# Optimization experiments

Measured on AMD Instinct MI355X. Metric: run time of the kernel, lower is better.

The kernel has to match this reference:

```python
import jax, jax.numpy as jnp
import numpy as np

HEADS = 8
DIM_HEAD = 64
QLEVEL = 127.0  # symmetric int8: clamp to [-128, 127]


def fake_quant(x):
    """Symmetric per-tensor int8 fake quantization with straight-through estimator."""
    delta = jnp.max(jnp.abs(x)) / QLEVEL
    xq = jnp.clip(jnp.round(x / delta), -128.0, 127.0) * delta
    return x + jax.lax.stop_gradient(xq - x)


def setup_inputs() -> dict:
    key = jax.random.key(0)
    ks = jax.random.split(key, 7)
    b, n, m, d, dc = 2, 4096, 1024, 512, 768
    return {
        "x": jax.random.normal(ks[0], (b, n, d), jnp.float32),
        "context": jax.random.normal(ks[1], (b, m, dc), jnp.float32),
        "Wq": jax.random.normal(ks[2], (d, d), jnp.float32) * 0.02,
        "Wk": jax.random.normal(ks[3], (dc, d), jnp.float32) * 0.02,
        "Wv": jax.random.normal(ks[4], (dc, d), jnp.float32) * 0.02,
        "Wo": jax.random.normal(ks[5], (d, d), jnp.float32) * 0.02,
        "bo": jnp.zeros((d,), jnp.float32),
    }


def reference(x, context, Wq, Wk, Wv, Wo, bo):
    b, n, _ = x.shape
    h, dh = HEADS, DIM_HEAD
    scale = dh ** -0.5

    q = x @ Wq            # [b, n, h*dh]
    k = context @ Wk      # [b, m, h*dh]
    v = context @ Wv      # [b, m, h*dh]

    def split(t):  # b n (h d) -> b h n d
        return t.reshape(t.shape[0], t.shape[1], h, dh).transpose(0, 2, 1, 3)

    q, k, v = split(q), split(k), split(v)

    # fake-quantize q and k before the score matmul (use_aq=True path)
    q = fake_quant(q)
    k = fake_quant(k)
    sim = jnp.einsum('bhid,bhjd->bhij', q, k) * scale  # [b, h, n, m]
    attn = jax.nn.softmax(sim, axis=-1)

    # fake-quantize attention weights and v before the AV matmul
    out = jnp.einsum('bhij,bhjd->bhid', fake_quant(attn), fake_quant(v))
    out = out.transpose(0, 2, 1, 3).reshape(b, n, h * dh)  # b h n d -> b n (h d)
    return out @ Wo + bo  # to_out[0]; to_out[-1] is Dropout (identity in eval)
```

## Files before the change

### kernel.cpp

```cpp
#include <hip/hip_runtime.h>
#include <stdint.h>

typedef float  v4f  __attribute__((ext_vector_type(4)));
typedef int    v4i  __attribute__((ext_vector_type(4)));
typedef __bf16 v8bf __attribute__((ext_vector_type(8)));
typedef __bf16 v4bf __attribute__((ext_vector_type(4)));

#define BATCH  2
#define NQ     4096
#define MK     1024
#define DMODEL 512
#define DCTX   768
#define NH     8
#define DH     64

__global__ __launch_bounds__(256) void k_wtrans(
    const float* __restrict__ Wq, const float* __restrict__ Wk,
    const float* __restrict__ Wv, const float* __restrict__ Wo,
    __bf16* __restrict__ Wq_t, __bf16* __restrict__ Wk_t,
    __bf16* __restrict__ Wv_t, __bf16* __restrict__ Wo_t,
    unsigned* __restrict__ scal) {
  if (blockIdx.x == 0 && blockIdx.y == 0 && blockIdx.z == 0 && threadIdx.x < 4)
    scal[threadIdx.x] = 0u;
  const float* src; __bf16* dst; int K;
  switch (blockIdx.z) {
    case 0:  src = Wq; dst = Wq_t; K = DMODEL; break;
    case 1:  src = Wk; dst = Wk_t; K = DCTX;   break;
    case 2:  src = Wv; dst = Wv_t; K = DCTX;   break;
    default: src = Wo; dst = Wo_t; K = DMODEL; break;
  }
  int k0 = blockIdx.y * 32;
  if (k0 >= K) return;
  int n0 = blockIdx.x * 32;
  __shared__ __bf16 tile[32][33];
  int c = threadIdx.x & 31, r0 = threadIdx.x >> 5;
  for (int i = 0; i < 4; ++i) {
    int r = r0 + i * 8;
    tile[c][r] = (__bf16)src[(size_t)(k0 + r) * DMODEL + n0 + c];
  }
  __syncthreads();
  for (int i = 0; i < 4; ++i) {
    int r = r0 + i * 8;
    dst[(size_t)(n0 + r) * K + k0 + c] = tile[r][c];
  }
}

__global__ __launch_bounds__(256) void k_cvt(
    const float* __restrict__ x, const float* __restrict__ ctx,
    __bf16* __restrict__ xb, __bf16* __restrict__ cb) {
  const int XC = BATCH * NQ * DMODEL / 8;
  const int CC = BATCH * MK * DCTX / 8;
  int idx = blockIdx.x * 256 + threadIdx.x;
  const float* src; __bf16* dst;
  if (idx < XC) { src = x + (size_t)idx * 8; dst = xb + (size_t)idx * 8; }
  else {
    int j = idx - XC;
    if (j >= CC) return;
    src = ctx + (size_t)j * 8; dst = cb + (size_t)j * 8;
  }
  float4 a = *(const float4*)src, b = *(const float4*)(src + 4);
  v8bf o = { (__bf16)a.x, (__bf16)a.y, (__bf16)a.z, (__bf16)a.w,
             (__bf16)b.x, (__bf16)b.y, (__bf16)b.z, (__bf16)b.w };
  *(v8bf*)dst = o;
}

template<int K_, bool BIAS, bool AMAX>
__global__ __launch_bounds__(256, 3) void k_gemm_bs(
    const __bf16* __restrict__ A, const __bf16* __restrict__ Bt,
    float* __restrict__ C, int M, int N,
    const float* __restrict__ bias,
    unsigned* __restrict__ amaxLo, unsigned* __restrict__ amaxHi) {
  constexpr int CS = K_ + 8;
  constexpr int GPC = K_ / 8;
  __shared__ __bf16 Bs[32 * CS];
  __shared__ float redmax[4];
  const int tid = threadIdx.x;
  const int lane = tid & 63, wave = tid >> 6;
  const int l15 = lane & 15, g = lane >> 4;
  const int col0 = blockIdx.y * 32;
  const int row0w = blockIdx.x * 128 + wave * 32;

#pragma unroll
  for (int i = 0; i < GPC * 32 / 256; ++i) {
    int f = i * 256 + tid;
    int c = f / GPC, w = f - c * GPC;
    *(v8bf*)(&Bs[c * CS + w * 8]) =
        *(const v8bf*)(Bt + (size_t)(col0 + c) * K_ + w * 8);
  }
  __syncthreads();

  v4f acc[2][2] = {};
  const __bf16* a0 = A + (size_t)(row0w + l15) * K_ + g * 8;
  const __bf16* a1 = A + (size_t)(row0w + 16 + l15) * K_ + g * 8;
#pragma unroll
  for (int k0 = 0; k0 < K_; k0 += 32) {
    v8bf af0 = *(const v8bf*)(a0 + k0);
    v8bf af1 = *(const v8bf*)(a1 + k0);
    v8bf bf0 = *(const v8bf*)(&Bs[l15 * CS + k0 + g * 8]);
    v8bf bf1 = *(const v8bf*)(&Bs[(16 + l15) * CS + k0 + g * 8]);
    acc[0][0] = __builtin_amdgcn_mfma_f32_16x16x32_bf16(af0, bf0, acc[0][0], 0, 0, 0);
    acc[0][1] = __builtin_amdgcn_mfma_f32_16x16x32_bf16(af0, bf1, acc[0][1], 0, 0, 0);
    acc[1][0] = __builtin_amdgcn_mfma_f32_16x16x32_bf16(af1, bf0, acc[1][0], 0, 0, 0);
    acc[1][1] = __builtin_amdgcn_mfma_f32_16x16x32_bf16(af1, bf1, acc[1][1], 0, 0, 0);
  }

  float lmax = 0.0f;
#pragma unroll
  for (int j = 0; j < 2; ++j) {
    int col = col0 + j * 16 + l15;
    float bv = BIAS ? bias[col] : 0.0f;
#pragma unroll
    for (int i = 0; i < 2; ++i) {
#pragma unroll
      for (int r = 0; r < 4; ++r) {
        int row = row0w + i * 16 + g * 4 + r;
        float cv = acc[i][j][r] + bv;
        C[(size_t)row * N + col] = cv;
        if (AMAX) lmax = fmaxf(lmax, fabsf(cv));
      }
    }
  }
  if (AMAX) {
    for (int off = 32; off > 0; off >>= 1)
      lmax = fmaxf(lmax, __shfl_xor(lmax, off, 64));
    if (lane == 0) redmax[wave] = lmax;
    __syncthreads();
    if (tid == 0) {
      float bm = fmaxf(fmaxf(redmax[0], redmax[1]), fmaxf(redmax[2], redmax[3]));
      atomicMax(col0 < 512 ? amaxLo : amaxHi, __float_as_uint(bm));
    }
  }
}

__global__ __launch_bounds__(256) void k_quant_kv(
    const float* __restrict__ kvf,
    int8_t* __restrict__ k8, int8_t* __restrict__ v8t,
    const unsigned* __restrict__ scal) {
  __shared__ int8_t tile[64][80];
  int bx = blockIdx.x;
  if (bx < 1024) {
    int j = bx * 256 + threadIdx.x;
    int r = j >> 7;
    int c4 = (j & 127) << 2;
    float4 v = *(const float4*)(kvf + (size_t)r * 1024 + c4);
    float s = 127.0f / __uint_as_float(scal[1]);
    int a0 = __float2int_rn(v.x * s), a1 = __float2int_rn(v.y * s);
    int a2 = __float2int_rn(v.z * s), a3 = __float2int_rn(v.w * s);
    a0 = max(-128, min(127, a0)); a1 = max(-128, min(127, a1));
    a2 = max(-128, min(127, a2)); a3 = max(-128, min(127, a3));
    unsigned p = (unsigned)(a0 & 255) | ((unsigned)(a1 & 255) << 8) |
                 ((unsigned)(a2 & 255) << 16) | ((unsigned)(a3 & 255) << 24);
    *(unsigned*)(k8 + (size_t)j * 4) = p;
    return;
  }
  int id = bx - 1024;
  int bh = id >> 4, b = bh >> 3, h = bh & 7;
  int j0 = (id & 15) * 64;
  const float s = 127.0f / __uint_as_float(scal[2]);
  int t = threadIdx.x;
  int j = t >> 2, dh0 = (t & 3) << 4;
  const float* src = kvf + (size_t)(b * MK + j0 + j) * 1024 + 512 + h * DH + dh0;
#pragma unroll
  for (int i = 0; i < 16; i += 4) {
    float4 v = *(const float4*)(src + i);
    int a0 = __float2int_rn(v.x * s), a1 = __float2int_rn(v.y * s);
    int a2 = __float2int_rn(v.z * s), a3 = __float2int_rn(v.w * s);
    tile[dh0 + i + 0][j] = (int8_t)max(-128, min(127, a0));
    tile[dh0 + i + 1][j] = (int8_t)max(-128, min(127, a1));
    tile[dh0 + i + 2][j] = (int8_t)max(-128, min(127, a2));
    tile[dh0 + i + 3][j] = (int8_t)max(-128, min(127, a3));
  }
  __syncthreads();
  int dh = t >> 2, jb = (t & 3) << 4;
  v4i val = *(const v4i*)(&tile[dh][jb]);
  *(v4i*)(v8t + (size_t)(bh * DH + dh) * MK + j0 + jb) = val;
}

__device__ __forceinline__ v4i quant_pack16(const float* p, float s) {
  v4i out;
#pragma unroll
  for (int q = 0; q < 4; ++q) {
    float4 v = *(const float4*)(p + q * 4);
    int a0 = __float2int_rn(v.x * s), a1 = __float2int_rn(v.y * s);
    int a2 = __float2int_rn(v.z * s), a3 = __float2int_rn(v.w * s);
    a0 = max(-128, min(127, a0)); a1 = max(-128, min(127, a1));
    a2 = max(-128, min(127, a2)); a3 = max(-128, min(127, a3));
    out[q] = (int)((unsigned)(a0 & 255) | ((unsigned)(a1 & 255) << 8) |
                   ((unsigned)(a2 & 255) << 16) | ((unsigned)(a3 & 255) << 24));
  }
  return out;
}

__global__ __launch_bounds__(256, 4) void k_pass1(
    const float* __restrict__ qf, int8_t* __restrict__ q8,
    const int8_t* __restrict__ k8,
    float* __restrict__ invz, unsigned* __restrict__ scal) {
  __shared__ __align__(16) int8_t kbuf[128 * 72];
  __shared__ float mared[4];
  int bh = blockIdx.y, b = bh >> 3, h = bh & 7;
  int wave = threadIdx.x >> 6, lane = threadIdx.x & 63;
  int l15 = lane & 15, g = lane >> 4;
  int row0 = blockIdx.x * 64;
  int myrow = row0 + wave * 16 + l15;
  const float aq = __uint_as_float(scal[0]), ak = __uint_as_float(scal[1]);
  const float alpha2 = (aq * ak) * (0.125f / (127.0f * 127.0f)) * 1.44269504f;
  const float sq = 127.0f / aq;
  const v4i z4 = {0, 0, 0, 0};
  size_t qoff = (size_t)(b * NQ + myrow) * DMODEL + h * DH + g * 16;
  v4i qfrag = quant_pack16(qf + qoff, sq);
  *(v4i*)(q8 + qoff) = qfrag;
  const int8_t* kbase = k8 + (size_t)b * MK * DMODEL + h * DH;
  const int rs = threadIdx.x >> 2, qs = (threadIdx.x & 3) * 16;

  float z[4] = {0.f, 0.f, 0.f, 0.f};
  int mi = -(1 << 30);
  for (int tile = 0; tile < 8; ++tile) {
    __syncthreads();
    *(v4i*)(&kbuf[rs * 72 + qs]) =
        *(const v4i*)(kbase + (size_t)(tile * 128 + rs) * DMODEL + qs);
    *(v4i*)(&kbuf[(rs + 64) * 72 + qs]) =
        *(const v4i*)(kbase + (size_t)(tile * 128 + rs + 64) * DMODEL + qs);
    __syncthreads();
    float zt = z[tile >> 1];
#pragma unroll
    for (int t = 0; t < 8; ++t) {
      v4i kfrag = *(const v4i*)(&kbuf[(t * 16 + l15) * 72 + g * 16]);
      v4i sa = __builtin_amdgcn_mfma_i32_16x16x64_i8(kfrag, qfrag, z4, 0, 0, 0);
      mi = max(mi, max(max(sa[0], sa[1]), max(sa[2], sa[3])));
      float e0 = __builtin_amdgcn_exp2f((float)sa[0] * alpha2);
      float e1 = __builtin_amdgcn_exp2f((float)sa[1] * alpha2);
      float e2 = __builtin_amdgcn_exp2f((float)sa[2] * alpha2);
      float e3 = __builtin_amdgcn_exp2f((float)sa[3] * alpha2);
      zt += (e0 + e1) + (e2 + e3);
    }
    z[tile >> 1] = zt;
  }
#pragma unroll
  for (int i = 0; i < 4; ++i) {
    z[i] += __shfl_xor(z[i], 16, 64);
    z[i] += __shfl_xor(z[i], 32, 64);
  }
  mi = max(mi, __shfl_xor(mi, 16, 64));
  mi = max(mi, __shfl_xor(mi, 32, 64));
  float zt = (z[0] + z[1]) + (z[2] + z[3]);
  float iz = 1.0f / zt;
  if (g == 0) invz[(size_t)bh * NQ + myrow] = iz;
  float ma = __builtin_amdgcn_exp2f((float)mi * alpha2) * iz;
#pragma unroll
  for (int off = 1; off < 16; off <<= 1)
    ma = fmaxf(ma, __shfl_xor(ma, off, 64));
  if (lane == 0) mared[wave] = ma;
  __syncthreads();
  if (threadIdx.x == 0)
    atomicMax(scal + 3,
              __float_as_uint(fmaxf(fmaxf(mared[0], mared[1]),
                                    fmaxf(mared[2], mared[3]))));
}

__global__ __launch_bounds__(256, 4) void k_pass2(
    const int8_t* __restrict__ q8, const int8_t* __restrict__ k8,
    const int8_t* __restrict__ v8t, const float* __restrict__ invz,
    const unsigned* __restrict__ scal, __bf16* __restrict__ o) {
  __shared__ __align__(16) int8_t kbuf[128 * 72];
  __shared__ __align__(16) int8_t vbuf[64 * 152];
  __shared__ __align__(16) int8_t albuf[4][16 * 152];
  int bh = blockIdx.y, b = bh >> 3, h = bh & 7;
  int wave = threadIdx.x >> 6, lane = threadIdx.x & 63;
  int l15 = lane & 15, g = lane >> 4;
  int row0 = blockIdx.x * 64;
  int myrow = row0 + wave * 16 + l15;
  const float aq = __uint_as_float(scal[0]), ak = __uint_as_float(scal[1]);
  const float avv = __uint_as_float(scal[2]), izm = __uint_as_float(scal[3]);
  const float alpha2 = (aq * ak) * (0.125f / (127.0f * 127.0f)) * 1.44269504f;
  const float oscale = (izm / 127.0f) * (avv / 127.0f);
  const float MAGIC = 12582912.0f;
  const v4i z4 = {0, 0, 0, 0};

  v4i qfrag = *(const v4i*)(q8 + (size_t)(b * NQ + myrow) * DMODEL + h * DH + g * 16);
  const float lcr = __builtin_amdgcn_logf(invz[(size_t)bh * NQ + myrow] * (127.0f / izm));
  const int8_t* kbase = k8 + (size_t)b * MK * DMODEL + h * DH;
  const int8_t* vbase = v8t + (size_t)bh * DH * MK;
  int8_t* alds = albuf[wave];
  const int rs = threadIdx.x >> 2, qs = (threadIdx.x & 3) * 16;
  const int vr = threadIdx.x >> 3, vq = (threadIdx.x & 7) * 16;

  v4i pacc[4] = {};
  for (int tile = 0; tile < 8; ++tile) {
    __syncthreads();
    *(v4i*)(&kbuf[rs * 72 + qs]) =
        *(const v4i*)(kbase + (size_t)(tile * 128 + rs) * DMODEL + qs);
    *(v4i*)(&kbuf[(rs + 64) * 72 + qs]) =
        *(const v4i*)(kbase + (size_t)(tile * 128 + rs + 64) * DMODEL + qs);
    *(v4i*)(&vbuf[vr * 152 + vq]) =
        *(const v4i*)(vbase + (size_t)vr * MK + tile * 128 + vq);
    *(v4i*)(&vbuf[(vr + 32) * 152 + vq]) =
        *(const v4i*)(vbase + (size_t)(vr + 32) * MK + tile * 128 + vq);
    __syncthreads();
#pragma unroll
    for (int t = 0; t < 8; ++t) {
      v4i kfrag = *(const v4i*)(&kbuf[(t * 16 + l15) * 72 + g * 16]);
      v4i sa = __builtin_amdgcn_mfma_i32_16x16x64_i8(kfrag, qfrag, z4, 0, 0, 0);
      float f0 = __builtin_amdgcn_exp2f(fmaf((float)sa[0], alpha2, lcr)) + MAGIC;
      float f1 = __builtin_amdgcn_exp2f(fmaf((float)sa[1], alpha2, lcr)) + MAGIC;
      float f2 = __builtin_amdgcn_exp2f(fmaf((float)sa[2], alpha2, lcr)) + MAGIC;
      float f3 = __builtin_amdgcn_exp2f(fmaf((float)sa[3], alpha2, lcr)) + MAGIC;
      unsigned packed = (__float_as_uint(f0) & 255u) |
                        ((__float_as_uint(f1) & 255u) << 8) |
                        ((__float_as_uint(f2) & 255u) << 16) |
                        (__float_as_uint(f3) << 24);
      *(unsigned*)(alds + l15 * 152 + t * 16 + g * 4) = packed;
    }
#pragma unroll
    for (int c = 0; c < 2; ++c) {
      v4i afrag = *(const v4i*)(alds + l15 * 152 + c * 64 + g * 16);
#pragma unroll
      for (int d = 0; d < 4; ++d) {
        v4i bfrag = *(const v4i*)(&vbuf[(d * 16 + l15) * 152 + c * 64 + g * 16]);
        pacc[d] = __builtin_amdgcn_mfma_i32_16x16x64_i8(afrag, bfrag, pacc[d], 0, 0, 0);
      }
    }
  }
  __bf16* obase = o + (size_t)(b * NQ + row0 + wave * 16) * DMODEL + h * DH;
#pragma unroll
  for (int d = 0; d < 4; ++d)
#pragma unroll
    for (int r = 0; r < 4; ++r)
      obase[(size_t)(g * 4 + r) * DMODEL + d * 16 + l15] =
          (__bf16)((float)pacc[d][r] * oscale);
}

extern "C" void kernel_launch(void* const* d_in, const int* in_sizes, int n_in,
                              void* d_out, int out_size, void* d_ws, size_t ws_size,
                              hipStream_t stream) {
  (void)in_sizes; (void)n_in; (void)out_size; (void)ws_size;
  const float* x   = (const float*)d_in[0];
  const float* ctx = (const float*)d_in[1];
  const float* Wq  = (const float*)d_in[2];
  const float* Wk  = (const float*)d_in[3];
  const float* Wv  = (const float*)d_in[4];
  const float* Wo  = (const float*)d_in[5];
  const float* bo  = (const float*)d_in[6];
  float* out = (float*)d_out;

  char* ws = (char*)d_ws;
  size_t off = 0;
  auto alloc = [&](size_t bytes) {
    char* p = ws + off;
    off += (bytes + 255) & ~(size_t)255;
    return p;
  };
  unsigned* scal = (unsigned*)alloc(16);
  __bf16* Wq_t = (__bf16*)alloc((size_t)512 * 512 * 2);
  __bf16* Wk_t = (__bf16*)alloc((size_t)512 * 768 * 2);
  __bf16* Wv_t = (__bf16*)alloc((size_t)512 * 768 * 2);
  __bf16* Wo_t = (__bf16*)alloc((size_t)512 * 512 * 2);
  __bf16* xb   = (__bf16*)alloc((size_t)BATCH * NQ * DMODEL * 2);
  __bf16* cb   = (__bf16*)alloc((size_t)BATCH * MK * DCTX * 2);
  float* qf  = (float*)alloc((size_t)BATCH * NQ * DMODEL * 4);
  float* kvf = (float*)alloc((size_t)BATCH * MK * 1024 * 4);
  int8_t* q8 = (int8_t*)alloc((size_t)BATCH * NQ * DMODEL);
  int8_t* k8 = (int8_t*)alloc((size_t)BATCH * MK * DMODEL);
  int8_t* v8t = (int8_t*)alloc((size_t)BATCH * NH * DH * MK);
  float* invz = (float*)alloc((size_t)BATCH * NH * NQ * 4);
  __bf16* o = (__bf16*)qf;

  k_wtrans<<<dim3(16, 24, 4), 256, 0, stream>>>(Wq, Wk, Wv, Wo, Wq_t, Wk_t, Wv_t, Wo_t, scal);
  k_cvt<<<2816, 256, 0, stream>>>(x, ctx, xb, cb);
  k_gemm_bs<512, false, true><<<dim3(64, 16), 256, 0, stream>>>(
      xb, Wq_t, qf, 8192, 512, nullptr, scal + 0, scal + 0);
  k_gemm_bs<768, false, true><<<dim3(16, 32), 256, 0, stream>>>(
      cb, Wk_t, kvf, 2048, 1024, nullptr, scal + 1, scal + 2);
  k_quant_kv<<<1280, 256, 0, stream>>>(kvf, k8, v8t, scal);
  k_pass1<<<dim3(64, 16), 256, 0, stream>>>(qf, q8, k8, invz, scal);
  k_pass2<<<dim3(64, 16), 256, 0, stream>>>(q8, k8, v8t, invz, scal, o);
  k_gemm_bs<512, true, false><<<dim3(64, 16), 256, 0, stream>>>(
      o, Wo_t, out, 8192, 512, bo, nullptr, nullptr);
}
```

Baseline: 201.8 us.

## Merge prep kernels and widen GEMM column tile to 64 for Q/out projections

Fuses the weight-transpose and input-conversion kernels into one launch, removing one kernel launch. The B-stationary GEMM gains a templated column-tile width; the Q and output projections now use 64-column tiles, so each A fragment feeds more MFMAs and A is re-read from global memory half as often. The price is doubled LDS for B (about 66KB at K=512), an occupancy hint lowered to 2, and half as many blocks.

```diff
diff --git a/kernel.cpp b/kernel.cpp
--- a/kernel.cpp
+++ b/kernel.cpp
@@ -14,24 +14,46 @@
 #define NH     8
 #define DH     64
 
-__global__ __launch_bounds__(256) void k_wtrans(
+__global__ __launch_bounds__(256) void k_prep(
+    const float* __restrict__ x, const float* __restrict__ ctx,
+    __bf16* __restrict__ xb, __bf16* __restrict__ cb,
     const float* __restrict__ Wq, const float* __restrict__ Wk,
     const float* __restrict__ Wv, const float* __restrict__ Wo,
     __bf16* __restrict__ Wq_t, __bf16* __restrict__ Wk_t,
     __bf16* __restrict__ Wv_t, __bf16* __restrict__ Wo_t,
     unsigned* __restrict__ scal) {
-  if (blockIdx.x == 0 && blockIdx.y == 0 && blockIdx.z == 0 && threadIdx.x < 4)
-    scal[threadIdx.x] = 0u;
+  int bx = blockIdx.x;
+  if (bx < 2816) {
+    const int XC = BATCH * NQ * DMODEL / 8;
+    const int CC = BATCH * MK * DCTX / 8;
+    int idx = bx * 256 + threadIdx.x;
+    const float* src; __bf16* dst;
+    if (idx < XC) { src = x + (size_t)idx * 8; dst = xb + (size_t)idx * 8; }
+    else {
+      int j = idx - XC;
+      if (j >= CC) return;
+      src = ctx + (size_t)j * 8; dst = cb + (size_t)j * 8;
+    }
+    float4 a = *(const float4*)src, b = *(const float4*)(src + 4);
+    v8bf o = { (__bf16)a.x, (__bf16)a.y, (__bf16)a.z, (__bf16)a.w,
+               (__bf16)b.x, (__bf16)b.y, (__bf16)b.z, (__bf16)b.w };
+    *(v8bf*)dst = o;
+    return;
+  }
+  int id = bx - 2816;
+  if (id == 0 && threadIdx.x < 4) scal[threadIdx.x] = 0u;
+  int tx = id & 15, rem = id >> 4;
+  int ty = rem % 24, tz = rem / 24;
   const float* src; __bf16* dst; int K;
-  switch (blockIdx.z) {
+  switch (tz) {
     case 0:  src = Wq; dst = Wq_t; K = DMODEL; break;
     case 1:  src = Wk; dst = Wk_t; K = DCTX;   break;
     case 2:  src = Wv; dst = Wv_t; K = DCTX;   break;
     default: src = Wo; dst = Wo_t; K = DMODEL; break;
   }
-  int k0 = blockIdx.y * 32;
+  int k0 = ty * 32;
   if (k0 >= K) return;
-  int n0 = blockIdx.x * 32;
+  int n0 = tx * 32;
   __shared__ __bf16 tile[32][33];
   int c = threadIdx.x & 31, r0 = threadIdx.x >> 5;
   for (int i = 0; i < 4; ++i) {
@@ -45,43 +67,25 @@
   }
 }
 
-__global__ __launch_bounds__(256) void k_cvt(
-    const float* __restrict__ x, const float* __restrict__ ctx,
-    __bf16* __restrict__ xb, __bf16* __restrict__ cb) {
-  const int XC = BATCH * NQ * DMODEL / 8;
-  const int CC = BATCH * MK * DCTX / 8;
-  int idx = blockIdx.x * 256 + threadIdx.x;
-  const float* src; __bf16* dst;
-  if (idx < XC) { src = x + (size_t)idx * 8; dst = xb + (size_t)idx * 8; }
-  else {
-    int j = idx - XC;
-    if (j >= CC) return;
-    src = ctx + (size_t)j * 8; dst = cb + (size_t)j * 8;
-  }
-  float4 a = *(const float4*)src, b = *(const float4*)(src + 4);
-  v8bf o = { (__bf16)a.x, (__bf16)a.y, (__bf16)a.z, (__bf16)a.w,
-             (__bf16)b.x, (__bf16)b.y, (__bf16)b.z, (__bf16)b.w };
-  *(v8bf*)dst = o;
-}
-
-template<int K_, bool BIAS, bool AMAX>
-__global__ __launch_bounds__(256, 3) void k_gemm_bs(
+template<int K_, int NC, bool BIAS, bool AMAX, int OCC>
+__global__ __launch_bounds__(256, OCC) void k_gemm_bs(
     const __bf16* __restrict__ A, const __bf16* __restrict__ Bt,
     float* __restrict__ C, int M, int N,
     const float* __restrict__ bias,
     unsigned* __restrict__ amaxLo, unsigned* __restrict__ amaxHi) {
   constexpr int CS = K_ + 8;
   constexpr int GPC = K_ / 8;
-  __shared__ __bf16 Bs[32 * CS];
+  constexpr int JT = NC / 16;
+  __shared__ __bf16 Bs[NC * CS];
   __shared__ float redmax[4];
   const int tid = threadIdx.x;
   const int lane = tid & 63, wave = tid >> 6;
   const int l15 = lane & 15, g = lane >> 4;
-  const int col0 = blockIdx.y * 32;
+  const int col0 = blockIdx.y * NC;
   const int row0w = blockIdx.x * 128 + wave * 32;
 
 #pragma unroll
-  for (int i = 0; i < GPC * 32 / 256; ++i) {
+  for (int i = 0; i < NC * GPC / 256; ++i) {
     int f = i * 256 + tid;
     int c = f / GPC, w = f - c * GPC;
     *(v8bf*)(&Bs[c * CS + w * 8]) =
@@ -89,24 +93,24 @@
   }
   __syncthreads();
 
-  v4f acc[2][2] = {};
+  v4f acc[2][JT] = {};
   const __bf16* a0 = A + (size_t)(row0w + l15) * K_ + g * 8;
   const __bf16* a1 = A + (size_t)(row0w + 16 + l15) * K_ + g * 8;
 #pragma unroll
   for (int k0 = 0; k0 < K_; k0 += 32) {
     v8bf af0 = *(const v8bf*)(a0 + k0);
     v8bf af1 = *(const v8bf*)(a1 + k0);
-    v8bf bf0 = *(const v8bf*)(&Bs[l15 * CS + k0 + g * 8]);
-    v8bf bf1 = *(const v8bf*)(&Bs[(16 + l15) * CS + k0 + g * 8]);
-    acc[0][0] = __builtin_amdgcn_mfma_f32_16x16x32_bf16(af0, bf0, acc[0][0], 0, 0, 0);
-    acc[0][1] = __builtin_amdgcn_mfma_f32_16x16x32_bf16(af0, bf1, acc[0][1], 0, 0, 0);
-    acc[1][0] = __builtin_amdgcn_mfma_f32_16x16x32_bf16(af1, bf0, acc[1][0], 0, 0, 0);
-    acc[1][1] = __builtin_amdgcn_mfma_f32_16x16x32_bf16(af1, bf1, acc[1][1], 0, 0, 0);
+#pragma unroll
+    for (int j = 0; j < JT; ++j) {
+      v8bf bfj = *(const v8bf*)(&Bs[(j * 16 + l15) * CS + k0 + g * 8]);
+      acc[0][j] = __builtin_amdgcn_mfma_f32_16x16x32_bf16(af0, bfj, acc[0][j], 0, 0, 0);
+      acc[1][j] = __builtin_amdgcn_mfma_f32_16x16x32_bf16(af1, bfj, acc[1][j], 0, 0, 0);
+    }
   }
 
   float lmax = 0.0f;
 #pragma unroll
-  for (int j = 0; j < 2; ++j) {
+  for (int j = 0; j < JT; ++j) {
     int col = col0 + j * 16 + l15;
     float bv = BIAS ? bias[col] : 0.0f;
 #pragma unroll
@@ -364,15 +368,15 @@
   float* invz = (float*)alloc((size_t)BATCH * NH * NQ * 4);
   __bf16* o = (__bf16*)qf;
 
-  k_wtrans<<<dim3(16, 24, 4), 256, 0, stream>>>(Wq, Wk, Wv, Wo, Wq_t, Wk_t, Wv_t, Wo_t, scal);
-  k_cvt<<<2816, 256, 0, stream>>>(x, ctx, xb, cb);
-  k_gemm_bs<512, false, true><<<dim3(64, 16), 256, 0, stream>>>(
+  k_prep<<<4352, 256, 0, stream>>>(x, ctx, xb, cb, Wq, Wk, Wv, Wo,
+                                   Wq_t, Wk_t, Wv_t, Wo_t, scal);
+  k_gemm_bs<512, 64, false, true, 2><<<dim3(64, 8), 256, 0, stream>>>(
       xb, Wq_t, qf, 8192, 512, nullptr, scal + 0, scal + 0);
-  k_gemm_bs<768, false, true><<<dim3(16, 32), 256, 0, stream>>>(
+  k_gemm_bs<768, 32, false, true, 3><<<dim3(16, 32), 256, 0, stream>>>(
       cb, Wk_t, kvf, 2048, 1024, nullptr, scal + 1, scal + 2);
   k_quant_kv<<<1280, 256, 0, stream>>>(kvf, k8, v8t, scal);
   k_pass1<<<dim3(64, 16), 256, 0, stream>>>(qf, q8, k8, invz, scal);
   k_pass2<<<dim3(64, 16), 256, 0, stream>>>(q8, k8, v8t, invz, scal, o);
-  k_gemm_bs<512, true, false><<<dim3(64, 16), 256, 0, stream>>>(
+  k_gemm_bs<512, 64, true, false, 2><<<dim3(64, 8), 256, 0, stream>>>(
       o, Wo_t, out, 8192, 512, bo, nullptr, nullptr);
 }
```

Measured after the change: 187.0 us. 1.08x faster.
